# Optimization experiments

Measured on AMD Instinct MI355X. Metric: run time of the kernel, lower is better.

## Reference

```python
import jax, jax.numpy as jnp
import numpy as np


def setup_inputs() -> dict:
    key = jax.random.key(0)
    k1, k2 = jax.random.split(key)
    B, N, M, D = 8, 4096, 4096, 128
    points1 = jax.random.normal(k1, (B, N, D), dtype=jnp.float32)
    points2 = jax.random.normal(k2, (B, M, D), dtype=jnp.float32)
    return {"points1": points1, "points2": points2}


def reference(points1, points2):
    # sum((x[:, :, None] - y[:, None, :])**2, -1), expressed as a GEMM).
    sq1 = jnp.sum(points1 * points1, axis=-1)              # [B, N]
    sq2 = jnp.sum(points2 * points2, axis=-1)              # [B, M]
    cross = jnp.einsum("bnd,bmd->bnm", points1, points2)   # [B, N, M]
    dist_matrix = sq1[:, :, None] + sq2[:, None, :] - 2.0 * cross
    min_dist1 = jnp.min(dist_matrix, axis=2)               # [B, N]
    min_dist2 = jnp.min(dist_matrix, axis=1)               # [B, M]
    return jnp.mean(min_dist1) + jnp.mean(min_dist2)
```

## Files before the change

### kernel.cpp

```cpp
#include <hip/hip_runtime.h>
#include <hip/hip_bf16.h>


#define BATCH 8
#define NPTS 4096
#define DIM 128
#define FBIAS 16384.0f

using bf16x8 = __attribute__((ext_vector_type(8))) short;
using f32x4  = __attribute__((ext_vector_type(4))) float;

__global__ void prep_kernel(const float* __restrict__ p1,
                            const float* __restrict__ p2,
                            __hip_bfloat16* __restrict__ b1,
                            __hip_bfloat16* __restrict__ b2,
                            float* __restrict__ s1,
                            float* __restrict__ s2) {
    const int arr = blockIdx.y;
    const float* src = arr ? p2 : p1;
    __hip_bfloat16* dst = arr ? b2 : b1;
    float* sq = arr ? s2 : s1;
    const float scale = arr ? 1.0f : -2.0f;

    const int wid = threadIdx.x >> 6;
    const int l   = threadIdx.x & 63;
    const int p   = blockIdx.x * 4 + wid;
    const float2 v = *reinterpret_cast<const float2*>(src + (size_t)p * DIM + l * 2);
    float s = v.x * v.x + v.y * v.y;
    __hip_bfloat162 h = __float22bfloat162_rn(make_float2(v.x * scale, v.y * scale));
    *reinterpret_cast<__hip_bfloat162*>(dst + (size_t)p * DIM + l * 2) = h;
    #pragma unroll
    for (int off = 1; off < 64; off <<= 1) s += __shfl_xor(s, off);
    if (l == 0) sq[p] = s;
}

__device__ __forceinline__ void stage16(const __hip_bfloat16* g, void* lds) {
    __builtin_amdgcn_global_load_lds(
        (const __attribute__((address_space(1))) void*)g,
        (__attribute__((address_space(3))) void*)lds, 16, 0, 0);
}

__global__ void __launch_bounds__(256, 4)
chamfer_tile_kernel(const __hip_bfloat16* __restrict__ bf1,
                    const __hip_bfloat16* __restrict__ bf2,
                    const float* __restrict__ sq1,
                    const float* __restrict__ sq2,
                    unsigned int* __restrict__ min1u,
                    unsigned int* __restrict__ min2u) {
    const int lin = blockIdx.x;
    const int b   = lin & 7;
    const int rest = lin >> 3;
    const int nt  = rest & 31;
    const int mh  = rest >> 5;
    const int tid = threadIdx.x;
    const int wid = tid >> 6;
    const int l   = tid & 63;
    const int l15 = l & 15;
    const int lhi = l >> 4;

    __shared__ __align__(16) unsigned char btile[2][64 * 256];
    __shared__ unsigned int colminu[1024];

    const __hip_bfloat16* bf1b = bf1 + (size_t)b * NPTS * DIM;
    const __hip_bfloat16* bf2b = bf2 + (size_t)b * NPTS * DIM;
    const float* sq2b = sq2 + b * NPTS;

    const int n0 = nt * 128 + wid * 32;

    bf16x8 afrag[2][4];
    #pragma unroll
    for (int rt = 0; rt < 2; ++rt)
        #pragma unroll
        for (int ks = 0; ks < 4; ++ks)
            afrag[rt][ks] = *reinterpret_cast<const bf16x8*>(
                bf1b + (n0 + rt * 16 + l15) * DIM + ks * 32 + lhi * 8);

    float sq1v[2][4];
    #pragma unroll
    for (int rt = 0; rt < 2; ++rt)
        #pragma unroll
        for (int j = 0; j < 4; ++j)
            sq1v[rt][j] = sq1[b * NPTS + n0 + rt * 16 + lhi * 4 + j];

    float rmin[2][4];
    #pragma unroll
    for (int rt = 0; rt < 2; ++rt)
        #pragma unroll
        for (int j = 0; j < 4; ++j) rmin[rt][j] = 3.4e38f;

    auto STAGE = [&](int buf, int m0) {
        #pragma unroll
        for (int j = 0; j < 4; ++j) {
            const int c   = j * 256 + wid * 64 + l;
            const int row = c >> 4;
            const int q   = c & 15;
            const __hip_bfloat16* src =
                bf2b + (size_t)(m0 + row) * DIM + (q ^ (row & 7)) * 8;
            stage16(src, &btile[buf][(j * 256 + wid * 64) * 16]);
        }
    };

    int cur = 0;
    STAGE(0, mh * 1024);
    #pragma unroll
    for (int i = 0; i < 4; ++i) colminu[i * 256 + tid] = 0xFFFFFFFFu;
    __syncthreads();

    for (int mt = 0; mt < 16; ++mt) {
        const int m0 = mh * 1024 + mt * 64;
        if (mt < 15) STAGE(cur ^ 1, m0 + 64);

        f32x4 acc[2][4];
        #pragma unroll
        for (int rt = 0; rt < 2; ++rt)
            #pragma unroll
            for (int ct = 0; ct < 4; ++ct) acc[rt][ct] = f32x4{0.f, 0.f, 0.f, 0.f};

        #pragma unroll
        for (int ks = 0; ks < 4; ++ks) {
            #pragma unroll
            for (int ct = 0; ct < 4; ++ct) {
                const int brow = ct * 16 + l15;
                const int kbyte = ks * 64 + lhi * 16;
                bf16x8 bfrag = *reinterpret_cast<const bf16x8*>(
                    &btile[cur][brow * 256 + (kbyte ^ ((brow & 7) << 4))]);
                #pragma unroll
                for (int rt = 0; rt < 2; ++rt)
                    acc[rt][ct] = __builtin_amdgcn_mfma_f32_16x16x32_bf16(
                        afrag[rt][ks], bfrag, acc[rt][ct], 0, 0, 0);
            }
        }

        float s2v[4];
        #pragma unroll
        for (int ct = 0; ct < 4; ++ct) s2v[ct] = sq2b[m0 + ct * 16 + l15];

        #pragma unroll
        for (int rt = 0; rt < 2; ++rt)
            #pragma unroll
            for (int j = 0; j < 4; ++j) {
                float r = rmin[rt][j];
                #pragma unroll
                for (int cp = 0; cp < 2; ++cp) {
                    const float t0 = acc[rt][2 * cp][j]     + s2v[2 * cp];
                    const float t1 = acc[rt][2 * cp + 1][j] + s2v[2 * cp + 1];
                    r = fminf(r, fminf(t0, t1));
                }
                rmin[rt][j] = r;
            }

        float cmin[4];
        #pragma unroll
        for (int ct = 0; ct < 4; ++ct) {
            float c = 3.4e38f;
            #pragma unroll
            for (int rt = 0; rt < 2; ++rt)
                #pragma unroll
                for (int jp = 0; jp < 2; ++jp) {
                    const float u0 = sq1v[rt][2 * jp]     + acc[rt][ct][2 * jp];
                    const float u1 = sq1v[rt][2 * jp + 1] + acc[rt][ct][2 * jp + 1];
                    c = fminf(c, fminf(u0, u1));
                }
            cmin[ct] = c;
        }

        #pragma unroll
        for (int ct = 0; ct < 4; ++ct) {
            cmin[ct] = fminf(cmin[ct], __shfl_xor(cmin[ct], 16));
            cmin[ct] = fminf(cmin[ct], __shfl_xor(cmin[ct], 32));
        }
        {
            float v = cmin[0];
            v = (lhi == 1) ? cmin[1] : v;
            v = (lhi == 2) ? cmin[2] : v;
            v = (lhi == 3) ? cmin[3] : v;
            atomicMin(&colminu[mt * 64 + l], __float_as_uint(v + FBIAS));
        }

        __syncthreads();
        cur ^= 1;
    }

    #pragma unroll
    for (int i = 0; i < 4; ++i) {
        const int c = i * 256 + tid;
        atomicMin(&min2u[(size_t)b * NPTS + mh * 1024 + c], colminu[c]);
    }

    #pragma unroll
    for (int rt = 0; rt < 2; ++rt)
        #pragma unroll
        for (int j = 0; j < 4; ++j) {
            float v = rmin[rt][j];
            v = fminf(v, __shfl_xor(v, 1));
            v = fminf(v, __shfl_xor(v, 2));
            v = fminf(v, __shfl_xor(v, 4));
            v = fminf(v, __shfl_xor(v, 8));
            rmin[rt][j] = v;
        }
    if (l15 == 0) {
        #pragma unroll
        for (int rt = 0; rt < 2; ++rt)
            #pragma unroll
            for (int j = 0; j < 4; ++j)
                atomicMin(&min1u[(size_t)b * NPTS + n0 + rt * 16 + lhi * 4 + j],
                          __float_as_uint(rmin[rt][j] + FBIAS));
    }
}

__global__ void finalize_kernel(const unsigned int* __restrict__ min1u,
                                const unsigned int* __restrict__ min2u,
                                const float* __restrict__ sq1,
                                const float* __restrict__ sq2,
                                float* __restrict__ out) {
    const int tid = threadIdx.x;
    const int gid = blockIdx.x * 256 + tid;
    float sum;

    if (gid < BATCH * NPTS) {
        sum = (__uint_as_float(min1u[gid]) - FBIAS + sq1[gid])
              * (1.0f / (BATCH * NPTS));
    } else {
        const int idx = gid - BATCH * NPTS;
        sum = (__uint_as_float(min2u[idx]) - FBIAS + sq2[idx])
              * (1.0f / (BATCH * NPTS));
    }

    #pragma unroll
    for (int off = 1; off < 64; off <<= 1) sum += __shfl_xor(sum, off);
    __shared__ float wsum[4];
    if ((tid & 63) == 0) wsum[tid >> 6] = sum;
    __syncthreads();
    if (tid == 0) atomicAdd(out, wsum[0] + wsum[1] + wsum[2] + wsum[3]);
}

extern "C" void kernel_launch(void* const* d_in, const int* in_sizes, int n_in,
                              void* d_out, int out_size, void* d_ws, size_t ws_size,
                              hipStream_t stream) {
    const float* p1 = (const float*)d_in[0];
    const float* p2 = (const float*)d_in[1];
    float* out = (float*)d_out;

    const size_t npts_tot = (size_t)BATCH * NPTS;
    __hip_bfloat16* bf1 = (__hip_bfloat16*)d_ws;
    __hip_bfloat16* bf2 = bf1 + npts_tot * DIM;
    float* sq1 = (float*)(bf2 + npts_tot * DIM);
    float* sq2 = sq1 + npts_tot;
    unsigned int* min1u = (unsigned int*)(sq2 + npts_tot);
    unsigned int* min2u = min1u + npts_tot;

    hipMemsetAsync(d_out, 0, sizeof(float), stream);
    hipMemsetAsync(min1u, 0xFF, npts_tot * 2 * sizeof(unsigned int), stream);

    prep_kernel<<<dim3(npts_tot / 4, 2), 256, 0, stream>>>(p1, p2, bf1, bf2, sq1, sq2);

    chamfer_tile_kernel<<<1024, 256, 0, stream>>>(bf1, bf2, sq1, sq2, min1u, min2u);

    finalize_kernel<<<256, 256, 0, stream>>>(min1u, min2u, sq1, sq2, out);
}
```

Baseline: 131.6 us.

## Software-pipeline column-min reduction and sq2 loads across tile iterations

Each iteration now runs the previous tile's cross-lane shuffle and LDS atomicMin step while the current tile's MFMAs are issued. The sq2 values are prefetched one tile ahead. The MFMA loop is reordered so each column pair's epilogue starts as soon as its accumulators finish. The aim is to hide shuffle, atomic and global-load latency behind matrix work. The cost is more live registers, which could reduce occupancy under the 4-blocks-per-SM launch bound.

```diff
diff --git a/kernel.cpp b/kernel.cpp
--- a/kernel.cpp
+++ b/kernel.cpp
@@ -57,6 +57,7 @@
     const int l   = tid & 63;
     const int l15 = l & 15;
     const int lhi = l >> 4;
+    const int base = mh * 1024;
 
     __shared__ __align__(16) unsigned char btile[2][64 * 256];
     __shared__ unsigned int colminu[1024];
@@ -100,91 +101,105 @@
         }
     };
 
+    auto TAIL = [&](const float* cp, int mtIdx) {
+        float c0 = fminf(cp[0], __shfl_xor(cp[0], 16));
+        float c1 = fminf(cp[1], __shfl_xor(cp[1], 16));
+        float c2 = fminf(cp[2], __shfl_xor(cp[2], 16));
+        float c3 = fminf(cp[3], __shfl_xor(cp[3], 16));
+        c0 = fminf(c0, __shfl_xor(c0, 32));
+        c1 = fminf(c1, __shfl_xor(c1, 32));
+        c2 = fminf(c2, __shfl_xor(c2, 32));
+        c3 = fminf(c3, __shfl_xor(c3, 32));
+        float v = c0;
+        v = (lhi == 1) ? c1 : v;
+        v = (lhi == 2) ? c2 : v;
+        v = (lhi == 3) ? c3 : v;
+        atomicMin(&colminu[mtIdx * 64 + l], __float_as_uint(v + FBIAS));
+    };
+
     int cur = 0;
-    STAGE(0, mh * 1024);
+    STAGE(0, base);
     #pragma unroll
     for (int i = 0; i < 4; ++i) colminu[i * 256 + tid] = 0xFFFFFFFFu;
+    float s2vN[4], s2vC[4];
+    #pragma unroll
+    for (int ct = 0; ct < 4; ++ct) s2vN[ct] = sq2b[base + ct * 16 + l15];
     __syncthreads();
 
+    float cminP[4];
+
     for (int mt = 0; mt < 16; ++mt) {
-        const int m0 = mh * 1024 + mt * 64;
+        const int m0 = base + mt * 64;
         if (mt < 15) STAGE(cur ^ 1, m0 + 64);
 
+        if (mt > 0) TAIL(cminP, mt - 1);
+
+        #pragma unroll
+        for (int ct = 0; ct < 4; ++ct) s2vC[ct] = s2vN[ct];
+        if (mt < 15) {
+            #pragma unroll
+            for (int ct = 0; ct < 4; ++ct)
+                s2vN[ct] = sq2b[m0 + 64 + ct * 16 + l15];
+        }
+
         f32x4 acc[2][4];
-        #pragma unroll
-        for (int rt = 0; rt < 2; ++rt)
-            #pragma unroll
-            for (int ct = 0; ct < 4; ++ct) acc[rt][ct] = f32x4{0.f, 0.f, 0.f, 0.f};
-
-        #pragma unroll
-        for (int ks = 0; ks < 4; ++ks) {
-            #pragma unroll
-            for (int ct = 0; ct < 4; ++ct) {
+        float cmin[4];
+        #pragma unroll
+        for (int cp = 0; cp < 2; ++cp) {
+            #pragma unroll
+            for (int cc = 0; cc < 2; ++cc) {
+                const int ct = 2 * cp + cc;
+                acc[0][ct] = f32x4{0.f, 0.f, 0.f, 0.f};
+                acc[1][ct] = f32x4{0.f, 0.f, 0.f, 0.f};
                 const int brow = ct * 16 + l15;
-                const int kbyte = ks * 64 + lhi * 16;
-                bf16x8 bfrag = *reinterpret_cast<const bf16x8*>(
-                    &btile[cur][brow * 256 + (kbyte ^ ((brow & 7) << 4))]);
+                #pragma unroll
+                for (int ks = 0; ks < 4; ++ks) {
+                    const int kbyte = ks * 64 + lhi * 16;
+                    bf16x8 bfrag = *reinterpret_cast<const bf16x8*>(
+                        &btile[cur][brow * 256 + (kbyte ^ ((brow & 7) << 4))]);
+                    #pragma unroll
+                    for (int rt = 0; rt < 2; ++rt)
+                        acc[rt][ct] = __builtin_amdgcn_mfma_f32_16x16x32_bf16(
+                            afrag[rt][ks], bfrag, acc[rt][ct], 0, 0, 0);
+                }
+            }
+            #pragma unroll
+            for (int rt = 0; rt < 2; ++rt)
+                #pragma unroll
+                for (int j = 0; j < 4; ++j) {
+                    const float t0 = acc[rt][2 * cp][j]     + s2vC[2 * cp];
+                    const float t1 = acc[rt][2 * cp + 1][j] + s2vC[2 * cp + 1];
+                    rmin[rt][j] = fminf(rmin[rt][j], fminf(t0, t1));
+                }
+            #pragma unroll
+            for (int cc = 0; cc < 2; ++cc) {
+                const int ct = 2 * cp + cc;
+                float c = 3.4e38f;
                 #pragma unroll
                 for (int rt = 0; rt < 2; ++rt)
-                    acc[rt][ct] = __builtin_amdgcn_mfma_f32_16x16x32_bf16(
-                        afrag[rt][ks], bfrag, acc[rt][ct], 0, 0, 0);
+                    #pragma unroll
+                    for (int jp = 0; jp < 2; ++jp) {
+                        const float u0 = sq1v[rt][2 * jp]     + acc[rt][ct][2 * jp];
+                        const float u1 = sq1v[rt][2 * jp + 1] + acc[rt][ct][2 * jp + 1];
+                        c = fminf(c, fminf(u0, u1));
+                    }
+                cmin[ct] = c;
             }
         }
-
-        float s2v[4];
-        #pragma unroll
-        for (int ct = 0; ct < 4; ++ct) s2v[ct] = sq2b[m0 + ct * 16 + l15];
-
-        #pragma unroll
-        for (int rt = 0; rt < 2; ++rt)
-            #pragma unroll
-            for (int j = 0; j < 4; ++j) {
-                float r = rmin[rt][j];
-                #pragma unroll
-                for (int cp = 0; cp < 2; ++cp) {
-                    const float t0 = acc[rt][2 * cp][j]     + s2v[2 * cp];
-                    const float t1 = acc[rt][2 * cp + 1][j] + s2v[2 * cp + 1];
-                    r = fminf(r, fminf(t0, t1));
-                }
-                rmin[rt][j] = r;
-            }
-
-        float cmin[4];
-        #pragma unroll
-        for (int ct = 0; ct < 4; ++ct) {
-            float c = 3.4e38f;
-            #pragma unroll
-            for (int rt = 0; rt < 2; ++rt)
-                #pragma unroll
-                for (int jp = 0; jp < 2; ++jp) {
-                    const float u0 = sq1v[rt][2 * jp]     + acc[rt][ct][2 * jp];
-                    const float u1 = sq1v[rt][2 * jp + 1] + acc[rt][ct][2 * jp + 1];
-                    c = fminf(c, fminf(u0, u1));
-                }
-            cmin[ct] = c;
-        }
-
-        #pragma unroll
-        for (int ct = 0; ct < 4; ++ct) {
-            cmin[ct] = fminf(cmin[ct], __shfl_xor(cmin[ct], 16));
-            cmin[ct] = fminf(cmin[ct], __shfl_xor(cmin[ct], 32));
-        }
-        {
-            float v = cmin[0];
-            v = (lhi == 1) ? cmin[1] : v;
-            v = (lhi == 2) ? cmin[2] : v;
-            v = (lhi == 3) ? cmin[3] : v;
-            atomicMin(&colminu[mt * 64 + l], __float_as_uint(v + FBIAS));
-        }
+        #pragma unroll
+        for (int ct = 0; ct < 4; ++ct) cminP[ct] = cmin[ct];
 
         __syncthreads();
         cur ^= 1;
     }
 
+    TAIL(cminP, 15);
+    __syncthreads();
+
     #pragma unroll
     for (int i = 0; i < 4; ++i) {
         const int c = i * 256 + tid;
-        atomicMin(&min2u[(size_t)b * NPTS + mh * 1024 + c], colminu[c]);
+        atomicMin(&min2u[(size_t)b * NPTS + base + c], colminu[c]);
     }
 
     #pragma unroll
```

Result: no change. 129.9 us (-1.3%).

## Switch to 32x32x16 MFMA tiles and defer column-min tail with manual barriers

Applied to the files above, without the earlier changes.

Replaces the 16x16x32 bf16 MFMA tiling with 32x32x16 MFMAs, so each wave does two large-accumulator MFMAs per k-step and issues fewer LDS fragment reads. The LDS swizzle is widened to 16 rows to match the new access pattern. The per-tile column-min atomics are deferred by one iteration and overlapped with the next tile's global-to-LDS staging. __syncthreads is replaced by raw s_barrier plus explicit vmcnt waits. The changed reduction shapes and hand-written synchronisation carry correctness and register-pressure risk.

```diff
diff --git a/kernel.cpp b/kernel.cpp
--- a/kernel.cpp
+++ b/kernel.cpp
@@ -8,7 +8,7 @@
 #define FBIAS 16384.0f
 
 using bf16x8 = __attribute__((ext_vector_type(8))) short;
-using f32x4  = __attribute__((ext_vector_type(4))) float;
+using f32x16 = __attribute__((ext_vector_type(16))) float;
 
 __global__ void prep_kernel(const float* __restrict__ p1,
                             const float* __restrict__ p2,
@@ -55,38 +55,37 @@
     const int tid = threadIdx.x;
     const int wid = tid >> 6;
     const int l   = tid & 63;
-    const int l15 = l & 15;
-    const int lhi = l >> 4;
+    const int l31 = l & 31;
+    const int lh  = l >> 5;
+    const int base = mh * 1024;
 
     __shared__ __align__(16) unsigned char btile[2][64 * 256];
     __shared__ unsigned int colminu[1024];
 
     const __hip_bfloat16* bf1b = bf1 + (size_t)b * NPTS * DIM;
     const __hip_bfloat16* bf2b = bf2 + (size_t)b * NPTS * DIM;
+    const float* sq1b = sq1 + b * NPTS;
     const float* sq2b = sq2 + b * NPTS;
 
     const int n0 = nt * 128 + wid * 32;
 
-    bf16x8 afrag[2][4];
-    #pragma unroll
-    for (int rt = 0; rt < 2; ++rt)
-        #pragma unroll
-        for (int ks = 0; ks < 4; ++ks)
-            afrag[rt][ks] = *reinterpret_cast<const bf16x8*>(
-                bf1b + (n0 + rt * 16 + l15) * DIM + ks * 32 + lhi * 8);
-
-    float sq1v[2][4];
-    #pragma unroll
-    for (int rt = 0; rt < 2; ++rt)
-        #pragma unroll
-        for (int j = 0; j < 4; ++j)
-            sq1v[rt][j] = sq1[b * NPTS + n0 + rt * 16 + lhi * 4 + j];
-
-    float rmin[2][4];
-    #pragma unroll
-    for (int rt = 0; rt < 2; ++rt)
-        #pragma unroll
-        for (int j = 0; j < 4; ++j) rmin[rt][j] = 3.4e38f;
+    bf16x8 afrag[8];
+    #pragma unroll
+    for (int ks = 0; ks < 8; ++ks)
+        afrag[ks] = *reinterpret_cast<const bf16x8*>(
+            bf1b + (n0 + l31) * DIM + ks * 16 + lh * 8);
+
+    float sq1v[16];
+    #pragma unroll
+    for (int reg = 0; reg < 16; ++reg)
+        sq1v[reg] = sq1b[n0 + (reg & 3) + 8 * (reg >> 2) + 4 * lh];
+
+    float rmin[16];
+    #pragma unroll
+    for (int reg = 0; reg < 16; ++reg) rmin[reg] = 3.4e38f;
+
+    const int bofs = l31 * 256 + ((lh * 16) ^ ((l & 1) << 4));
+    const int vks  = (l & 14) << 4;
 
     auto STAGE = [&](int buf, int m0) {
         #pragma unroll
@@ -95,116 +94,92 @@
             const int row = c >> 4;
             const int q   = c & 15;
             const __hip_bfloat16* src =
-                bf2b + (size_t)(m0 + row) * DIM + (q ^ (row & 7)) * 8;
-            stage16(src, &btile[buf][(j * 256 + wid * 64) * 16]);
+                bf2b + (size_t)(m0 + row) * DIM + (q ^ (row & 15)) * 8;
+            stage16(src, &btile[buf][c * 16]);
         }
     };
 
+    auto TAIL = [&](float cp0, float cp1, int mtIdx) {
+        float v0 = fminf(cp0, __shfl_xor(cp0, 32));
+        float v1 = fminf(cp1, __shfl_xor(cp1, 32));
+        if (l < 32) {
+            atomicMin(&colminu[mtIdx * 64 + l], __float_as_uint(v0 + FBIAS));
+            atomicMin(&colminu[mtIdx * 64 + 32 + l], __float_as_uint(v1 + FBIAS));
+        }
+    };
+
+    #pragma unroll
+    for (int i = 0; i < 4; ++i) colminu[i * 256 + tid] = 0xFFFFFFFFu;
+    STAGE(0, base);
+
+    float cp0 = 3.4e38f, cp1 = 3.4e38f;
     int cur = 0;
-    STAGE(0, mh * 1024);
-    #pragma unroll
-    for (int i = 0; i < 4; ++i) colminu[i * 256 + tid] = 0xFFFFFFFFu;
+
+    for (int mt = 0; mt < 16; ++mt) {
+        const int m0 = base + mt * 64;
+
+        asm volatile("s_barrier" ::: "memory");
+        if (mt < 15) STAGE(cur ^ 1, m0 + 64);
+        if (mt > 0)  TAIL(cp0, cp1, mt - 1);
+        if (mt < 15) asm volatile("s_waitcnt vmcnt(4)\n\ts_barrier" ::: "memory");
+        else         asm volatile("s_waitcnt vmcnt(0)\n\ts_barrier" ::: "memory");
+
+        f32x16 acc0 = {}, acc1 = {};
+        const unsigned char* bt = &btile[cur][0];
+        #pragma unroll
+        for (int ks = 0; ks < 8; ++ks) {
+            const int ko = ((ks * 32) ^ vks);
+            bf16x8 b0 = *reinterpret_cast<const bf16x8*>(&bt[bofs + ko]);
+            bf16x8 b1 = *reinterpret_cast<const bf16x8*>(&bt[bofs + ko + 8192]);
+            acc0 = __builtin_amdgcn_mfma_f32_32x32x16_bf16(afrag[ks], b0, acc0, 0, 0, 0);
+            acc1 = __builtin_amdgcn_mfma_f32_32x32x16_bf16(afrag[ks], b1, acc1, 0, 0, 0);
+        }
+
+        const float s2v0 = sq2b[m0 + l31];
+        const float s2v1 = sq2b[m0 + 32 + l31];
+        #pragma unroll
+        for (int reg = 0; reg < 16; ++reg)
+            rmin[reg] = fminf(rmin[reg],
+                              fminf(acc0[reg] + s2v0, acc1[reg] + s2v1));
+
+        float c0 = 3.4e38f, c1 = 3.4e38f;
+        #pragma unroll
+        for (int reg = 0; reg < 16; reg += 2) {
+            c0 = fminf(c0, fminf(acc0[reg] + sq1v[reg],
+                                 acc0[reg + 1] + sq1v[reg + 1]));
+            c1 = fminf(c1, fminf(acc1[reg] + sq1v[reg],
+                                 acc1[reg + 1] + sq1v[reg + 1]));
+        }
+        cp0 = c0; cp1 = c1;
+        cur ^= 1;
+    }
+
+    TAIL(cp0, cp1, 15);
     __syncthreads();
-
-    for (int mt = 0; mt < 16; ++mt) {
-        const int m0 = mh * 1024 + mt * 64;
-        if (mt < 15) STAGE(cur ^ 1, m0 + 64);
-
-        f32x4 acc[2][4];
-        #pragma unroll
-        for (int rt = 0; rt < 2; ++rt)
-            #pragma unroll
-            for (int ct = 0; ct < 4; ++ct) acc[rt][ct] = f32x4{0.f, 0.f, 0.f, 0.f};
-
-        #pragma unroll
-        for (int ks = 0; ks < 4; ++ks) {
-            #pragma unroll
-            for (int ct = 0; ct < 4; ++ct) {
-                const int brow = ct * 16 + l15;
-                const int kbyte = ks * 64 + lhi * 16;
-                bf16x8 bfrag = *reinterpret_cast<const bf16x8*>(
-                    &btile[cur][brow * 256 + (kbyte ^ ((brow & 7) << 4))]);
-                #pragma unroll
-                for (int rt = 0; rt < 2; ++rt)
-                    acc[rt][ct] = __builtin_amdgcn_mfma_f32_16x16x32_bf16(
-                        afrag[rt][ks], bfrag, acc[rt][ct], 0, 0, 0);
-            }
-        }
-
-        float s2v[4];
-        #pragma unroll
-        for (int ct = 0; ct < 4; ++ct) s2v[ct] = sq2b[m0 + ct * 16 + l15];
-
-        #pragma unroll
-        for (int rt = 0; rt < 2; ++rt)
-            #pragma unroll
-            for (int j = 0; j < 4; ++j) {
-                float r = rmin[rt][j];
-                #pragma unroll
-                for (int cp = 0; cp < 2; ++cp) {
-                    const float t0 = acc[rt][2 * cp][j]     + s2v[2 * cp];
-                    const float t1 = acc[rt][2 * cp + 1][j] + s2v[2 * cp + 1];
-                    r = fminf(r, fminf(t0, t1));
-                }
-                rmin[rt][j] = r;
-            }
-
-        float cmin[4];
-        #pragma unroll
-        for (int ct = 0; ct < 4; ++ct) {
-            float c = 3.4e38f;
-            #pragma unroll
-            for (int rt = 0; rt < 2; ++rt)
-                #pragma unroll
-                for (int jp = 0; jp < 2; ++jp) {
-                    const float u0 = sq1v[rt][2 * jp]     + acc[rt][ct][2 * jp];
-                    const float u1 = sq1v[rt][2 * jp + 1] + acc[rt][ct][2 * jp + 1];
-                    c = fminf(c, fminf(u0, u1));
-                }
-            cmin[ct] = c;
-        }
-
-        #pragma unroll
-        for (int ct = 0; ct < 4; ++ct) {
-            cmin[ct] = fminf(cmin[ct], __shfl_xor(cmin[ct], 16));
-            cmin[ct] = fminf(cmin[ct], __shfl_xor(cmin[ct], 32));
-        }
-        {
-            float v = cmin[0];
-            v = (lhi == 1) ? cmin[1] : v;
-            v = (lhi == 2) ? cmin[2] : v;
-            v = (lhi == 3) ? cmin[3] : v;
-            atomicMin(&colminu[mt * 64 + l], __float_as_uint(v + FBIAS));
-        }
-
-        __syncthreads();
-        cur ^= 1;
-    }
 
     #pragma unroll
     for (int i = 0; i < 4; ++i) {
         const int c = i * 256 + tid;
-        atomicMin(&min2u[(size_t)b * NPTS + mh * 1024 + c], colminu[c]);
-    }
-
-    #pragma unroll
-    for (int rt = 0; rt < 2; ++rt)
-        #pragma unroll
-        for (int j = 0; j < 4; ++j) {
-            float v = rmin[rt][j];
-            v = fminf(v, __shfl_xor(v, 1));
-            v = fminf(v, __shfl_xor(v, 2));
-            v = fminf(v, __shfl_xor(v, 4));
-            v = fminf(v, __shfl_xor(v, 8));
-            rmin[rt][j] = v;
-        }
-    if (l15 == 0) {
-        #pragma unroll
-        for (int rt = 0; rt < 2; ++rt)
-            #pragma unroll
-            for (int j = 0; j < 4; ++j)
-                atomicMin(&min1u[(size_t)b * NPTS + n0 + rt * 16 + lhi * 4 + j],
-                          __float_as_uint(rmin[rt][j] + FBIAS));
+        atomicMin(&min2u[(size_t)b * NPTS + base + c], colminu[c]);
+    }
+
+    #pragma unroll
+    for (int reg = 0; reg < 16; ++reg) {
+        float v = rmin[reg];
+        v = fminf(v, __shfl_xor(v, 1));
+        v = fminf(v, __shfl_xor(v, 2));
+        v = fminf(v, __shfl_xor(v, 4));
+        v = fminf(v, __shfl_xor(v, 8));
+        v = fminf(v, __shfl_xor(v, 16));
+        rmin[reg] = v;
+    }
+    if (l31 == 0) {
+        #pragma unroll
+        for (int reg = 0; reg < 16; ++reg) {
+            const int row = n0 + (reg & 3) + 8 * (reg >> 2) + 4 * lh;
+            atomicMin(&min1u[(size_t)b * NPTS + row],
+                      __float_as_uint(rmin[reg] + FBIAS));
+        }
     }
 }
 
```

Measured after the change: 138.8 us. 1.05x slower.
